# Kernel optimization log

Hardware: AMD Instinct MI355X
Metric: run time of the kernel (lower is better)

## Reference

```python
import jax, jax.numpy as jnp
import numpy as np

ALIGN_CORNERS = True
APPLY_SMOOTHSTEP = True

SIZES = [(32, 32, 32), (64, 64, 64), (128, 128, 128), (256, 256, 256)]
FEAT_DIMS = [4, 4, 4, 4]
N_POINTS = 1048576  # 2**20 sample points (e.g. 8192 rays x 128 samples)


def setup_inputs() -> dict:
    key = jax.random.key(0)
    ks = jax.random.split(key, 1 + len(SIZES))
    # grid_sample-style coords in [-1, 1], layout [1, 1, 1, N, 3] (x, y, z)
    grid = jax.random.uniform(ks[0], (1, 1, 1, N_POINTS, 3), dtype=jnp.float32) * 2.0 - 1.0
    inp = {"grid": grid}
    for i, (size, c) in enumerate(zip(SIZES, FEAT_DIMS)):
        # original init: (rand(1,C,1,1,1)*2-1).repeat over spatial; use randn volumes for a
        # non-degenerate baseline (same shapes/math path)
        inp[f"vol{i}"] = jax.random.normal(ks[1 + i], (1, c, *size), dtype=jnp.float32)
    return inp


def _smooth_sample(vol, grid_pts):
    """Trilinear sample with border padding, align_corners=True, smoothstep weights.

    vol: [C, D, H, W]; grid_pts: [P, 3] with (x, y, z) in [-1, 1].
    Returns [C, P].
    """
    C, D, H, W = vol.shape
    # unnormalize (align_corners=True): [-1,1] -> [0, dim-1]; border padding via clip
    x = jnp.clip((grid_pts[:, 0] + 1.0) * 0.5 * (W - 1), 0.0, W - 1)
    y = jnp.clip((grid_pts[:, 1] + 1.0) * 0.5 * (H - 1), 0.0, H - 1)
    z = jnp.clip((grid_pts[:, 2] + 1.0) * 0.5 * (D - 1), 0.0, D - 1)

    x0 = jnp.floor(x); y0 = jnp.floor(y); z0 = jnp.floor(z)
    tx = x - x0; ty = y - y0; tz = z - z0
    if APPLY_SMOOTHSTEP:
        tx = tx * tx * (3.0 - 2.0 * tx)
        ty = ty * ty * (3.0 - 2.0 * ty)
        tz = tz * tz * (3.0 - 2.0 * tz)

    x0i = x0.astype(jnp.int32); x1i = jnp.minimum(x0i + 1, W - 1)
    y0i = y0.astype(jnp.int32); y1i = jnp.minimum(y0i + 1, H - 1)
    z0i = z0.astype(jnp.int32); z1i = jnp.minimum(z0i + 1, D - 1)

    # 8 corner gathers -> [C, P]
    c000 = vol[:, z0i, y0i, x0i]; c001 = vol[:, z0i, y0i, x1i]
    c010 = vol[:, z0i, y1i, x0i]; c011 = vol[:, z0i, y1i, x1i]
    c100 = vol[:, z1i, y0i, x0i]; c101 = vol[:, z1i, y0i, x1i]
    c110 = vol[:, z1i, y1i, x0i]; c111 = vol[:, z1i, y1i, x1i]

    c00 = c000 + (c001 - c000) * tx
    c01 = c010 + (c011 - c010) * tx
    c10 = c100 + (c101 - c100) * tx
    c11 = c110 + (c111 - c110) * tx
    c0 = c00 + (c01 - c00) * ty
    c1 = c10 + (c11 - c10) * ty
    return c0 + (c1 - c0) * tz


def reference(grid, vol0, vol1, vol2, vol3):
    # grid: [1, 1, 1, N, 3] -> [N, 3]
    pts = grid.reshape(-1, 3)
    n = pts.shape[0]
    out = []
    for vol in (vol0, vol1, vol2, vol3):
        feat = _smooth_sample(vol[0], pts)            # [C, N]
        out.append(feat.reshape(1, -1, 1, 1, n))      # grid_sample output layout
    return jnp.concatenate(out, axis=1)               # [1, sum(C), 1, 1, N]
```

## Files before the change

kernel.cpp:

```cpp
#include <hip/hip_runtime.h>

#define NPTS 1048576
#define NB 32
#define NBINS (NB * NB * NB)

typedef float v4f __attribute__((ext_vector_type(4)));

__device__ __forceinline__ void nt_store4(const float4& f, float4* p) {
    __builtin_nontemporal_store(*(const v4f*)&f, (v4f*)p);
}


__device__ __forceinline__ float4 lerp4(const float4 a, const float4 b, const float t) {
    return make_float4(a.x + (b.x - a.x) * t,
                       a.y + (b.y - a.y) * t,
                       a.z + (b.z - a.z) * t,
                       a.w + (b.w - a.w) * t);
}

struct CoordW { float tx, ty, tz; int b00, b01, b10, b11, x0, x1; };

template<int D>
__device__ __forceinline__ CoordW mkcoord(float gx, float gy, float gz) {
    CoordW c;
    float x = fminf(fmaxf((gx + 1.0f) * (0.5f * (float)(D - 1)), 0.0f), (float)(D - 1));
    float y = fminf(fmaxf((gy + 1.0f) * (0.5f * (float)(D - 1)), 0.0f), (float)(D - 1));
    float z = fminf(fmaxf((gz + 1.0f) * (0.5f * (float)(D - 1)), 0.0f), (float)(D - 1));
    float xf = floorf(x), yf = floorf(y), zf = floorf(z);
    float tx = x - xf, ty = y - yf, tz = z - zf;
    c.tx = tx * tx * (3.0f - 2.0f * tx);
    c.ty = ty * ty * (3.0f - 2.0f * ty);
    c.tz = tz * tz * (3.0f - 2.0f * tz);
    int x0 = (int)xf, y0 = (int)yf, z0 = (int)zf;
    int y1 = min(y0 + 1, D - 1), z1 = min(z0 + 1, D - 1);
    c.x0 = x0;
    c.x1 = min(x0 + 1, D - 1);
    c.b00 = (z0 * D + y0) * D;
    c.b01 = (z0 * D + y1) * D;
    c.b10 = (z1 * D + y0) * D;
    c.b11 = (z1 * D + y1) * D;
    return c;
}

__device__ __forceinline__ float4 reduce8(const float4* q, const CoordW& c) {
    float4 c00 = lerp4(q[0], q[1], c.tx);
    float4 c01 = lerp4(q[2], q[3], c.tx);
    float4 c10 = lerp4(q[4], q[5], c.tx);
    float4 c11 = lerp4(q[6], q[7], c.tx);
    float4 c0 = lerp4(c00, c01, c.ty);
    float4 c1 = lerp4(c10, c11, c.ty);
    return lerp4(c0, c1, c.tz);
}


#define DHW0 (32 * 32 * 32)
#define DHW1 (64 * 64 * 64)
#define DHW2 (128 * 128 * 128)

__global__ __launch_bounds__(256) void xpose_all_kernel(
    const float* __restrict__ v0, const float* __restrict__ v1, const float* __restrict__ v2,
    float4* __restrict__ w0, float4* __restrict__ w1, float4* __restrict__ w2)
{
    constexpr int B2 = DHW2 / 256, B1 = DHW1 / 256;
    int b = blockIdx.x;
    int t = threadIdx.x;
    if (b < B2) {
        int v = b * 256 + t;
        w2[v] = make_float4(v2[v], v2[v + DHW2], v2[v + 2 * DHW2], v2[v + 3 * DHW2]);
    } else if (b < B2 + B1) {
        int v = (b - B2) * 256 + t;
        w1[v] = make_float4(v1[v], v1[v + DHW1], v1[v + 2 * DHW1], v1[v + 3 * DHW1]);
    } else {
        int v = (b - B2 - B1) * 256 + t;
        w0[v] = make_float4(v0[v], v0[v + DHW0], v0[v + 2 * DHW0], v0[v + 3 * DHW0]);
    }
}


__device__ __forceinline__ int bin_of(float gx, float gy, float gz) {
    float ux = fminf(fmaxf((gx + 1.0f) * 0.5f, 0.0f), 1.0f);
    float uy = fminf(fmaxf((gy + 1.0f) * 0.5f, 0.0f), 1.0f);
    float uz = fminf(fmaxf((gz + 1.0f) * 0.5f, 0.0f), 1.0f);
    int bx = min((int)(ux * (float)NB), NB - 1);
    int by = min((int)(uy * (float)NB), NB - 1);
    int bz = min((int)(uz * (float)NB), NB - 1);
    return (bz * NB + by) * NB + bx;
}

__global__ __launch_bounds__(256) void bin_hist_kernel(const float* __restrict__ grid,
                                                       unsigned* __restrict__ hist) {
    int p = blockIdx.x * blockDim.x + threadIdx.x;
    float gx = grid[3 * p + 0];
    float gy = grid[3 * p + 1];
    float gz = grid[3 * p + 2];
    atomicAdd(&hist[bin_of(gx, gy, gz)], 1u);
}

__global__ __launch_bounds__(1024) void scan_kernel(const unsigned* __restrict__ hist,
                                                    unsigned* __restrict__ offsets) {
    __shared__ unsigned partial[1024];
    const int t = threadIdx.x;
    const int base = t * 32;
    unsigned sum = 0;
#pragma unroll
    for (int i = 0; i < 32; ++i) sum += hist[base + i];
    partial[t] = sum;
    __syncthreads();
    for (int off = 1; off < 1024; off <<= 1) {
        unsigned v = (t >= off) ? partial[t - off] : 0u;
        __syncthreads();
        partial[t] += v;
        __syncthreads();
    }
    unsigned run = partial[t] - sum;
#pragma unroll
    for (int i = 0; i < 32; ++i) {
        offsets[base + i] = run;
        run += hist[base + i];
    }
}

__global__ __launch_bounds__(256) void scatter_kernel(const float* __restrict__ grid,
                                                      unsigned* __restrict__ offsets,
                                                      float4* __restrict__ sorted,
                                                      int* __restrict__ inv) {
    int p = blockIdx.x * blockDim.x + threadIdx.x;
    float gx = grid[3 * p + 0];
    float gy = grid[3 * p + 1];
    float gz = grid[3 * p + 2];
    int b = bin_of(gx, gy, gz);
    unsigned pos = atomicAdd(&offsets[b], 1u);
    sorted[pos] = make_float4(gx, gy, gz, __int_as_float(p));
    inv[p] = (int)pos;
}


__global__ __launch_bounds__(256, 4) void gather_sorted_kernel(
    const float4* __restrict__ sorted,
    const float4* __restrict__ w0, const float4* __restrict__ w1,
    const float4* __restrict__ w2, const float* __restrict__ v3,
    float4* __restrict__ wsout)
{
    int bid = blockIdx.x;
    int sb = (bid & 7) * (int)(gridDim.x >> 3) + (bid >> 3);
    int s = sb * 256 + (int)threadIdx.x;
    float4 gp = sorted[s];
    float gx = gp.x, gy = gp.y, gz = gp.z;

    CoordW c0 = mkcoord<32>(gx, gy, gz);
    CoordW c1 = mkcoord<64>(gx, gy, gz);
    CoordW c2 = mkcoord<128>(gx, gy, gz);
    CoordW c3 = mkcoord<256>(gx, gy, gz);

    float4 qa[8], qb[8], qc[8];
    qa[0] = w0[c0.b00 + c0.x0]; qa[1] = w0[c0.b00 + c0.x1];
    qa[2] = w0[c0.b01 + c0.x0]; qa[3] = w0[c0.b01 + c0.x1];
    qa[4] = w0[c0.b10 + c0.x0]; qa[5] = w0[c0.b10 + c0.x1];
    qa[6] = w0[c0.b11 + c0.x0]; qa[7] = w0[c0.b11 + c0.x1];

    qb[0] = w1[c1.b00 + c1.x0]; qb[1] = w1[c1.b00 + c1.x1];
    qb[2] = w1[c1.b01 + c1.x0]; qb[3] = w1[c1.b01 + c1.x1];
    qb[4] = w1[c1.b10 + c1.x0]; qb[5] = w1[c1.b10 + c1.x1];
    qb[6] = w1[c1.b11 + c1.x0]; qb[7] = w1[c1.b11 + c1.x1];

    qc[0] = w2[c2.b00 + c2.x0]; qc[1] = w2[c2.b00 + c2.x1];
    qc[2] = w2[c2.b01 + c2.x0]; qc[3] = w2[c2.b01 + c2.x1];
    qc[4] = w2[c2.b10 + c2.x0]; qc[5] = w2[c2.b10 + c2.x1];
    qc[6] = w2[c2.b11 + c2.x0]; qc[7] = w2[c2.b11 + c2.x1];

    const int xm = min(c3.x0, 254);
    const bool edge = (c3.x0 == 255);
    float2 qd[16];
#pragma unroll
    for (int ch = 0; ch < 4; ++ch) {
        const float* __restrict__ vc = v3 + (size_t)ch * (256 * 256 * 256);
        qd[ch * 4 + 0] = *(const float2*)(vc + c3.b00 + xm);
        qd[ch * 4 + 1] = *(const float2*)(vc + c3.b01 + xm);
        qd[ch * 4 + 2] = *(const float2*)(vc + c3.b10 + xm);
        qd[ch * 4 + 3] = *(const float2*)(vc + c3.b11 + xm);
    }

    float4 f0 = reduce8(qa, c0);
    float4 f1 = reduce8(qb, c1);
    float4 f2 = reduce8(qc, c2);

    float r3[4];
#pragma unroll
    for (int ch = 0; ch < 4; ++ch) {
        float v00a = edge ? qd[ch * 4 + 0].y : qd[ch * 4 + 0].x, v00b = qd[ch * 4 + 0].y;
        float v01a = edge ? qd[ch * 4 + 1].y : qd[ch * 4 + 1].x, v01b = qd[ch * 4 + 1].y;
        float v10a = edge ? qd[ch * 4 + 2].y : qd[ch * 4 + 2].x, v10b = qd[ch * 4 + 2].y;
        float v11a = edge ? qd[ch * 4 + 3].y : qd[ch * 4 + 3].x, v11b = qd[ch * 4 + 3].y;
        float c00 = v00a + (v00b - v00a) * c3.tx;
        float c01 = v01a + (v01b - v01a) * c3.tx;
        float c10 = v10a + (v10b - v10a) * c3.tx;
        float c11 = v11a + (v11b - v11a) * c3.tx;
        float e0 = c00 + (c01 - c00) * c3.ty;
        float e1 = c10 + (c11 - c10) * c3.ty;
        r3[ch] = e0 + (e1 - e0) * c3.tz;
    }
    float4 f3 = make_float4(r3[0], r3[1], r3[2], r3[3]);

    float4* w = wsout + (size_t)s * 4;
    nt_store4(f0, w + 0);
    nt_store4(f1, w + 1);
    nt_store4(f2, w + 2);
    nt_store4(f3, w + 3);
}


__device__ __forceinline__ void permute_one(const float4* __restrict__ wsout,
                                            const int* __restrict__ inv,
                                            float* __restrict__ out, int p) {
    int s = inv[p];
    const float4* w = wsout + (size_t)s * 4;
    float4 f0 = w[0], f1 = w[1], f2 = w[2], f3 = w[3];
    __builtin_nontemporal_store(f0.x, &out[ 0 * NPTS + p]);
    __builtin_nontemporal_store(f0.y, &out[ 1 * NPTS + p]);
    __builtin_nontemporal_store(f0.z, &out[ 2 * NPTS + p]);
    __builtin_nontemporal_store(f0.w, &out[ 3 * NPTS + p]);
    __builtin_nontemporal_store(f1.x, &out[ 4 * NPTS + p]);
    __builtin_nontemporal_store(f1.y, &out[ 5 * NPTS + p]);
    __builtin_nontemporal_store(f1.z, &out[ 6 * NPTS + p]);
    __builtin_nontemporal_store(f1.w, &out[ 7 * NPTS + p]);
    __builtin_nontemporal_store(f2.x, &out[ 8 * NPTS + p]);
    __builtin_nontemporal_store(f2.y, &out[ 9 * NPTS + p]);
    __builtin_nontemporal_store(f2.z, &out[10 * NPTS + p]);
    __builtin_nontemporal_store(f2.w, &out[11 * NPTS + p]);
    __builtin_nontemporal_store(f3.x, &out[12 * NPTS + p]);
    __builtin_nontemporal_store(f3.y, &out[13 * NPTS + p]);
    __builtin_nontemporal_store(f3.z, &out[14 * NPTS + p]);
    __builtin_nontemporal_store(f3.w, &out[15 * NPTS + p]);
}

__global__ __launch_bounds__(256) void permute_kernel(const float4* __restrict__ wsout,
                                                      const int* __restrict__ inv,
                                                      float* __restrict__ out) {
    int p = blockIdx.x * blockDim.x + threadIdx.x;
    permute_one(wsout, inv, out, p);
    permute_one(wsout, inv, out, p + NPTS / 2);
}


template<int D>
__device__ __forceinline__ float4 sample_inter(const float4* __restrict__ v,
                                               float gx, float gy, float gz) {
    CoordW c = mkcoord<D>(gx, gy, gz);
    float4 q[8];
    q[0] = v[c.b00 + c.x0]; q[1] = v[c.b00 + c.x1];
    q[2] = v[c.b01 + c.x0]; q[3] = v[c.b01 + c.x1];
    q[4] = v[c.b10 + c.x0]; q[5] = v[c.b10 + c.x1];
    q[6] = v[c.b11 + c.x0]; q[7] = v[c.b11 + c.x1];
    return reduce8(q, c);
}

template<int D>
__device__ __forceinline__ float4 sample_direct(const float* __restrict__ v,
                                                float gx, float gy, float gz) {
    CoordW c = mkcoord<D>(gx, gy, gz);
    float r[4];
#pragma unroll
    for (int ch = 0; ch < 4; ++ch) {
        const float* __restrict__ vc = v + (size_t)ch * (D * D * D);
        float c000 = vc[c.b00 + c.x0], c001 = vc[c.b00 + c.x1];
        float c010 = vc[c.b01 + c.x0], c011 = vc[c.b01 + c.x1];
        float c100 = vc[c.b10 + c.x0], c101 = vc[c.b10 + c.x1];
        float c110 = vc[c.b11 + c.x0], c111 = vc[c.b11 + c.x1];
        float c00 = c000 + (c001 - c000) * c.tx;
        float c01 = c010 + (c011 - c010) * c.tx;
        float c10 = c100 + (c101 - c100) * c.tx;
        float c11 = c110 + (c111 - c110) * c.tx;
        float e0 = c00 + (c01 - c00) * c.ty;
        float e1 = c10 + (c11 - c10) * c.ty;
        r[ch] = e0 + (e1 - e0) * c.tz;
    }
    return make_float4(r[0], r[1], r[2], r[3]);
}

__global__ __launch_bounds__(256) void mg_direct_kernel(
    const float* __restrict__ grid,
    const float* __restrict__ v0, const float* __restrict__ v1,
    const float* __restrict__ v2, const float* __restrict__ v3,
    float* __restrict__ out)
{
    int p = blockIdx.x * blockDim.x + threadIdx.x;
    float gx = grid[3 * p + 0];
    float gy = grid[3 * p + 1];
    float gz = grid[3 * p + 2];
    float4 f0 = sample_direct<32>(v0, gx, gy, gz);
    float4 f1 = sample_direct<64>(v1, gx, gy, gz);
    float4 f2 = sample_direct<128>(v2, gx, gy, gz);
    float4 f3 = sample_direct<256>(v3, gx, gy, gz);
    out[ 0 * NPTS + p] = f0.x; out[ 1 * NPTS + p] = f0.y;
    out[ 2 * NPTS + p] = f0.z; out[ 3 * NPTS + p] = f0.w;
    out[ 4 * NPTS + p] = f1.x; out[ 5 * NPTS + p] = f1.y;
    out[ 6 * NPTS + p] = f1.z; out[ 7 * NPTS + p] = f1.w;
    out[ 8 * NPTS + p] = f2.x; out[ 9 * NPTS + p] = f2.y;
    out[10 * NPTS + p] = f2.z; out[11 * NPTS + p] = f2.w;
    out[12 * NPTS + p] = f3.x; out[13 * NPTS + p] = f3.y;
    out[14 * NPTS + p] = f3.z; out[15 * NPTS + p] = f3.w;
}

__global__ __launch_bounds__(256) void mg_inter_kernel(
    const float* __restrict__ grid,
    const float4* __restrict__ w0, const float4* __restrict__ w1,
    const float4* __restrict__ w2, const float* __restrict__ v3,
    float* __restrict__ out)
{
    int p = blockIdx.x * blockDim.x + threadIdx.x;
    float gx = grid[3 * p + 0];
    float gy = grid[3 * p + 1];
    float gz = grid[3 * p + 2];
    float4 f0 = sample_inter<32>(w0, gx, gy, gz);
    float4 f1 = sample_inter<64>(w1, gx, gy, gz);
    float4 f2 = sample_inter<128>(w2, gx, gy, gz);
    float4 f3 = sample_direct<256>(v3, gx, gy, gz);
    out[ 0 * NPTS + p] = f0.x; out[ 1 * NPTS + p] = f0.y;
    out[ 2 * NPTS + p] = f0.z; out[ 3 * NPTS + p] = f0.w;
    out[ 4 * NPTS + p] = f1.x; out[ 5 * NPTS + p] = f1.y;
    out[ 6 * NPTS + p] = f1.z; out[ 7 * NPTS + p] = f1.w;
    out[ 8 * NPTS + p] = f2.x; out[ 9 * NPTS + p] = f2.y;
    out[10 * NPTS + p] = f2.z; out[11 * NPTS + p] = f2.w;
    out[12 * NPTS + p] = f3.x; out[13 * NPTS + p] = f3.y;
    out[14 * NPTS + p] = f3.z; out[15 * NPTS + p] = f3.w;
}


extern "C" void kernel_launch(void* const* d_in, const int* in_sizes, int n_in,
                              void* d_out, int out_size, void* d_ws, size_t ws_size,
                              hipStream_t stream) {
    const float* grid = (const float*)d_in[0];
    const float* v0   = (const float*)d_in[1];
    const float* v1   = (const float*)d_in[2];
    const float* v2   = (const float*)d_in[3];
    const float* v3   = (const float*)d_in[4];
    float* out = (float*)d_out;

    constexpr size_t OFF_WSOUT  = 0;
    constexpr size_t OFF_SORTED = OFF_WSOUT  + (size_t)NPTS * 64;
    constexpr size_t OFF_W2     = OFF_SORTED + (size_t)NPTS * 16;
    constexpr size_t OFF_W1     = OFF_W2     + (size_t)DHW2 * 16;
    constexpr size_t OFF_W0     = OFF_W1     + (size_t)DHW1 * 16;
    constexpr size_t OFF_INV    = OFF_W0     + (size_t)DHW0 * 16;
    constexpr size_t OFF_HIST   = OFF_INV    + (size_t)NPTS * 4;
    constexpr size_t OFF_OFFS   = OFF_HIST   + (size_t)NBINS * 4;
    constexpr size_t WS_FULL    = OFF_OFFS   + (size_t)NBINS * 4;
    constexpr size_t WS_INTER   = (size_t)(DHW0 + DHW1 + DHW2) * 16;

    const int threads = 256;
    const int pt_blocks = NPTS / threads;
    char* ws = (char*)d_ws;

    if (ws_size >= WS_FULL) {
        float4*   wsout  = (float4*)(ws + OFF_WSOUT);
        float4*   sorted = (float4*)(ws + OFF_SORTED);
        float4*   w2     = (float4*)(ws + OFF_W2);
        float4*   w1     = (float4*)(ws + OFF_W1);
        float4*   w0     = (float4*)(ws + OFF_W0);
        int*      inv    = (int*)   (ws + OFF_INV);
        unsigned* hist   = (unsigned*)(ws + OFF_HIST);
        unsigned* offs   = (unsigned*)(ws + OFF_OFFS);

        (void)hipMemsetAsync(hist, 0, (size_t)NBINS * 4, stream);
        xpose_all_kernel<<<(DHW0 + DHW1 + DHW2) / threads, threads, 0, stream>>>(
            v0, v1, v2, w0, w1, w2);
        bin_hist_kernel<<<pt_blocks, threads, 0, stream>>>(grid, hist);
        scan_kernel<<<1, 1024, 0, stream>>>(hist, offs);
        scatter_kernel<<<pt_blocks, threads, 0, stream>>>(grid, offs, sorted, inv);
        gather_sorted_kernel<<<pt_blocks, threads, 0, stream>>>(sorted, w0, w1, w2, v3, wsout);
        permute_kernel<<<pt_blocks / 2, threads, 0, stream>>>(wsout, inv, out);
    } else if (ws_size >= WS_INTER) {
        float4* w0 = (float4*)d_ws;
        float4* w1 = w0 + DHW0;
        float4* w2 = w1 + DHW1;
        xpose_all_kernel<<<(DHW0 + DHW1 + DHW2) / threads, threads, 0, stream>>>(
            v0, v1, v2, w0, w1, w2);
        mg_inter_kernel<<<pt_blocks, threads, 0, stream>>>(grid, w0, w1, w2, v3, out);
    } else {
        mg_direct_kernel<<<pt_blocks, threads, 0, stream>>>(grid, v0, v1, v2, v3, out);
    }
}
```

Measured before the change: 662.8 us.

## Fuse transpose with histogram, split gather output into per-level SoA buffers

Merges the volume transpose and point histogram kernels into one launch to cut a kernel launch and let the two independent workloads overlap. The gather kernel now writes each level's float4 into a separate structure-of-arrays buffer right after its reduction, with a scheduling barrier placed after all loads, and its occupancy hint drops from 4 to 3 waves. The permute kernel issues both points' inv and workspace loads before any stores. These changes aim to cut launch overhead and improve memory-level parallelism, at the cost of higher register pressure and less coalesced per-level reads in the permute.

```diff
diff --git a/kernel.cpp b/kernel.cpp
--- a/kernel.cpp
+++ b/kernel.cpp
@@ -3,6 +3,10 @@
 #define NPTS 1048576
 #define NB 32
 #define NBINS (NB * NB * NB)
+
+#define DHW0 (32 * 32 * 32)
+#define DHW1 (64 * 64 * 64)
+#define DHW2 (128 * 128 * 128)
 
 typedef float v4f __attribute__((ext_vector_type(4)));
 
@@ -53,15 +57,23 @@
 }
 
 
-#define DHW0 (32 * 32 * 32)
-#define DHW1 (64 * 64 * 64)
-#define DHW2 (128 * 128 * 128)
-
-__global__ __launch_bounds__(256) void xpose_all_kernel(
+__device__ __forceinline__ int bin_of(float gx, float gy, float gz) {
+    float ux = fminf(fmaxf((gx + 1.0f) * 0.5f, 0.0f), 1.0f);
+    float uy = fminf(fmaxf((gy + 1.0f) * 0.5f, 0.0f), 1.0f);
+    float uz = fminf(fmaxf((gz + 1.0f) * 0.5f, 0.0f), 1.0f);
+    int bx = min((int)(ux * (float)NB), NB - 1);
+    int by = min((int)(uy * (float)NB), NB - 1);
+    int bz = min((int)(uz * (float)NB), NB - 1);
+    return (bz * NB + by) * NB + bx;
+}
+
+
+__global__ __launch_bounds__(256) void xpose_hist_kernel(
     const float* __restrict__ v0, const float* __restrict__ v1, const float* __restrict__ v2,
-    float4* __restrict__ w0, float4* __restrict__ w1, float4* __restrict__ w2)
+    float4* __restrict__ w0, float4* __restrict__ w1, float4* __restrict__ w2,
+    const float* __restrict__ grid, unsigned* __restrict__ hist)
 {
-    constexpr int B2 = DHW2 / 256, B1 = DHW1 / 256;
+    constexpr int B2 = DHW2 / 256, B1 = DHW1 / 256, B0 = DHW0 / 256;
     int b = blockIdx.x;
     int t = threadIdx.x;
     if (b < B2) {
@@ -70,30 +82,16 @@
     } else if (b < B2 + B1) {
         int v = (b - B2) * 256 + t;
         w1[v] = make_float4(v1[v], v1[v + DHW1], v1[v + 2 * DHW1], v1[v + 3 * DHW1]);
-    } else {
+    } else if (b < B2 + B1 + B0) {
         int v = (b - B2 - B1) * 256 + t;
         w0[v] = make_float4(v0[v], v0[v + DHW0], v0[v + 2 * DHW0], v0[v + 3 * DHW0]);
-    }
-}
-
-
-__device__ __forceinline__ int bin_of(float gx, float gy, float gz) {
-    float ux = fminf(fmaxf((gx + 1.0f) * 0.5f, 0.0f), 1.0f);
-    float uy = fminf(fmaxf((gy + 1.0f) * 0.5f, 0.0f), 1.0f);
-    float uz = fminf(fmaxf((gz + 1.0f) * 0.5f, 0.0f), 1.0f);
-    int bx = min((int)(ux * (float)NB), NB - 1);
-    int by = min((int)(uy * (float)NB), NB - 1);
-    int bz = min((int)(uz * (float)NB), NB - 1);
-    return (bz * NB + by) * NB + bx;
-}
-
-__global__ __launch_bounds__(256) void bin_hist_kernel(const float* __restrict__ grid,
-                                                       unsigned* __restrict__ hist) {
-    int p = blockIdx.x * blockDim.x + threadIdx.x;
-    float gx = grid[3 * p + 0];
-    float gy = grid[3 * p + 1];
-    float gz = grid[3 * p + 2];
-    atomicAdd(&hist[bin_of(gx, gy, gz)], 1u);
+    } else {
+        int p = (b - B2 - B1 - B0) * 256 + t;
+        float gx = grid[3 * p + 0];
+        float gy = grid[3 * p + 1];
+        float gz = grid[3 * p + 2];
+        atomicAdd(&hist[bin_of(gx, gy, gz)], 1u);
+    }
 }
 
 __global__ __launch_bounds__(1024) void scan_kernel(const unsigned* __restrict__ hist,
@@ -135,11 +133,12 @@
 }
 
 
-__global__ __launch_bounds__(256, 4) void gather_sorted_kernel(
+__global__ __launch_bounds__(256, 3) void gather_sorted_kernel(
     const float4* __restrict__ sorted,
     const float4* __restrict__ w0, const float4* __restrict__ w1,
     const float4* __restrict__ w2, const float* __restrict__ v3,
-    float4* __restrict__ wsout)
+    float4* __restrict__ ws0, float4* __restrict__ ws1,
+    float4* __restrict__ ws2, float4* __restrict__ ws3)
 {
     int bid = blockIdx.x;
     int sb = (bid & 7) * (int)(gridDim.x >> 3) + (bid >> 3);
@@ -151,8 +150,12 @@
     CoordW c1 = mkcoord<64>(gx, gy, gz);
     CoordW c2 = mkcoord<128>(gx, gy, gz);
     CoordW c3 = mkcoord<256>(gx, gy, gz);
+    const int xm = min(c3.x0, 254);
+    const bool edge = (c3.x0 == 255);
 
     float4 qa[8], qb[8], qc[8];
+    float2 qd[16];
+
     qa[0] = w0[c0.b00 + c0.x0]; qa[1] = w0[c0.b00 + c0.x1];
     qa[2] = w0[c0.b01 + c0.x0]; qa[3] = w0[c0.b01 + c0.x1];
     qa[4] = w0[c0.b10 + c0.x0]; qa[5] = w0[c0.b10 + c0.x1];
@@ -168,9 +171,6 @@
     qc[4] = w2[c2.b10 + c2.x0]; qc[5] = w2[c2.b10 + c2.x1];
     qc[6] = w2[c2.b11 + c2.x0]; qc[7] = w2[c2.b11 + c2.x1];
 
-    const int xm = min(c3.x0, 254);
-    const bool edge = (c3.x0 == 255);
-    float2 qd[16];
 #pragma unroll
     for (int ch = 0; ch < 4; ++ch) {
         const float* __restrict__ vc = v3 + (size_t)ch * (256 * 256 * 256);
@@ -180,9 +180,14 @@
         qd[ch * 4 + 3] = *(const float2*)(vc + c3.b11 + xm);
     }
 
+    __builtin_amdgcn_sched_barrier(0);
+
     float4 f0 = reduce8(qa, c0);
+    nt_store4(f0, ws0 + s);
     float4 f1 = reduce8(qb, c1);
+    nt_store4(f1, ws1 + s);
     float4 f2 = reduce8(qc, c2);
+    nt_store4(f2, ws2 + s);
 
     float r3[4];
 #pragma unroll
@@ -200,21 +205,16 @@
         r3[ch] = e0 + (e1 - e0) * c3.tz;
     }
     float4 f3 = make_float4(r3[0], r3[1], r3[2], r3[3]);
-
-    float4* w = wsout + (size_t)s * 4;
-    nt_store4(f0, w + 0);
-    nt_store4(f1, w + 1);
-    nt_store4(f2, w + 2);
-    nt_store4(f3, w + 3);
-}
-
-
-__device__ __forceinline__ void permute_one(const float4* __restrict__ wsout,
-                                            const int* __restrict__ inv,
-                                            float* __restrict__ out, int p) {
-    int s = inv[p];
-    const float4* w = wsout + (size_t)s * 4;
-    float4 f0 = w[0], f1 = w[1], f2 = w[2], f3 = w[3];
+    nt_store4(f3, ws3 + s);
+}
+
+
+__device__ __forceinline__ void permute_one(const float4* __restrict__ ws0,
+                                            const float4* __restrict__ ws1,
+                                            const float4* __restrict__ ws2,
+                                            const float4* __restrict__ ws3,
+                                            int s, float* __restrict__ out, int p) {
+    float4 f0 = ws0[s], f1 = ws1[s], f2 = ws2[s], f3 = ws3[s];
     __builtin_nontemporal_store(f0.x, &out[ 0 * NPTS + p]);
     __builtin_nontemporal_store(f0.y, &out[ 1 * NPTS + p]);
     __builtin_nontemporal_store(f0.z, &out[ 2 * NPTS + p]);
@@ -233,12 +233,56 @@
     __builtin_nontemporal_store(f3.w, &out[15 * NPTS + p]);
 }
 
-__global__ __launch_bounds__(256) void permute_kernel(const float4* __restrict__ wsout,
-                                                      const int* __restrict__ inv,
-                                                      float* __restrict__ out) {
+__global__ __launch_bounds__(256) void permute_kernel(
+    const float4* __restrict__ ws0, const float4* __restrict__ ws1,
+    const float4* __restrict__ ws2, const float4* __restrict__ ws3,
+    const int* __restrict__ inv, float* __restrict__ out) {
     int p = blockIdx.x * blockDim.x + threadIdx.x;
-    permute_one(wsout, inv, out, p);
-    permute_one(wsout, inv, out, p + NPTS / 2);
+    int sA = inv[p];
+    int sB = inv[p + NPTS / 2];
+    float4 a0 = ws0[sA], a1 = ws1[sA], a2 = ws2[sA], a3 = ws3[sA];
+    float4 b0 = ws0[sB], b1 = ws1[sB], b2 = ws2[sB], b3 = ws3[sB];
+    __builtin_amdgcn_sched_barrier(0);
+    {
+        float4 f0 = a0, f1 = a1, f2 = a2, f3 = a3;
+        int q = p;
+        __builtin_nontemporal_store(f0.x, &out[ 0 * NPTS + q]);
+        __builtin_nontemporal_store(f0.y, &out[ 1 * NPTS + q]);
+        __builtin_nontemporal_store(f0.z, &out[ 2 * NPTS + q]);
+        __builtin_nontemporal_store(f0.w, &out[ 3 * NPTS + q]);
+        __builtin_nontemporal_store(f1.x, &out[ 4 * NPTS + q]);
+        __builtin_nontemporal_store(f1.y, &out[ 5 * NPTS + q]);
+        __builtin_nontemporal_store(f1.z, &out[ 6 * NPTS + q]);
+        __builtin_nontemporal_store(f1.w, &out[ 7 * NPTS + q]);
+        __builtin_nontemporal_store(f2.x, &out[ 8 * NPTS + q]);
+        __builtin_nontemporal_store(f2.y, &out[ 9 * NPTS + q]);
+        __builtin_nontemporal_store(f2.z, &out[10 * NPTS + q]);
+        __builtin_nontemporal_store(f2.w, &out[11 * NPTS + q]);
+        __builtin_nontemporal_store(f3.x, &out[12 * NPTS + q]);
+        __builtin_nontemporal_store(f3.y, &out[13 * NPTS + q]);
+        __builtin_nontemporal_store(f3.z, &out[14 * NPTS + q]);
+        __builtin_nontemporal_store(f3.w, &out[15 * NPTS + q]);
+    }
+    {
+        float4 f0 = b0, f1 = b1, f2 = b2, f3 = b3;
+        int q = p + NPTS / 2;
+        __builtin_nontemporal_store(f0.x, &out[ 0 * NPTS + q]);
+        __builtin_nontemporal_store(f0.y, &out[ 1 * NPTS + q]);
+        __builtin_nontemporal_store(f0.z, &out[ 2 * NPTS + q]);
+        __builtin_nontemporal_store(f0.w, &out[ 3 * NPTS + q]);
+        __builtin_nontemporal_store(f1.x, &out[ 4 * NPTS + q]);
+        __builtin_nontemporal_store(f1.y, &out[ 5 * NPTS + q]);
+        __builtin_nontemporal_store(f1.z, &out[ 6 * NPTS + q]);
+        __builtin_nontemporal_store(f1.w, &out[ 7 * NPTS + q]);
+        __builtin_nontemporal_store(f2.x, &out[ 8 * NPTS + q]);
+        __builtin_nontemporal_store(f2.y, &out[ 9 * NPTS + q]);
+        __builtin_nontemporal_store(f2.z, &out[10 * NPTS + q]);
+        __builtin_nontemporal_store(f2.w, &out[11 * NPTS + q]);
+        __builtin_nontemporal_store(f3.x, &out[12 * NPTS + q]);
+        __builtin_nontemporal_store(f3.y, &out[13 * NPTS + q]);
+        __builtin_nontemporal_store(f3.z, &out[14 * NPTS + q]);
+        __builtin_nontemporal_store(f3.w, &out[15 * NPTS + q]);
+    }
 }
 
 
@@ -352,7 +396,10 @@
     char* ws = (char*)d_ws;
 
     if (ws_size >= WS_FULL) {
-        float4*   wsout  = (float4*)(ws + OFF_WSOUT);
+        float4*   ws0    = (float4*)(ws + OFF_WSOUT);
+        float4*   ws1    = ws0 + NPTS;
+        float4*   ws2    = ws0 + 2 * (size_t)NPTS;
+        float4*   ws3    = ws0 + 3 * (size_t)NPTS;
         float4*   sorted = (float4*)(ws + OFF_SORTED);
         float4*   w2     = (float4*)(ws + OFF_W2);
         float4*   w1     = (float4*)(ws + OFF_W1);
@@ -362,19 +409,20 @@
         unsigned* offs   = (unsigned*)(ws + OFF_OFFS);
 
         (void)hipMemsetAsync(hist, 0, (size_t)NBINS * 4, stream);
-        xpose_all_kernel<<<(DHW0 + DHW1 + DHW2) / threads, threads, 0, stream>>>(
-            v0, v1, v2, w0, w1, w2);
-        bin_hist_kernel<<<pt_blocks, threads, 0, stream>>>(grid, hist);
+        const int xh_blocks = (DHW0 + DHW1 + DHW2) / threads + pt_blocks;
+        xpose_hist_kernel<<<xh_blocks, threads, 0, stream>>>(
+            v0, v1, v2, w0, w1, w2, grid, hist);
         scan_kernel<<<1, 1024, 0, stream>>>(hist, offs);
         scatter_kernel<<<pt_blocks, threads, 0, stream>>>(grid, offs, sorted, inv);
-        gather_sorted_kernel<<<pt_blocks, threads, 0, stream>>>(sorted, w0, w1, w2, v3, wsout);
-        permute_kernel<<<pt_blocks / 2, threads, 0, stream>>>(wsout, inv, out);
+        gather_sorted_kernel<<<pt_blocks, threads, 0, stream>>>(
+            sorted, w0, w1, w2, v3, ws0, ws1, ws2, ws3);
+        permute_kernel<<<pt_blocks / 2, threads, 0, stream>>>(ws0, ws1, ws2, ws3, inv, out);
     } else if (ws_size >= WS_INTER) {
         float4* w0 = (float4*)d_ws;
         float4* w1 = w0 + DHW0;
         float4* w2 = w1 + DHW1;
-        xpose_all_kernel<<<(DHW0 + DHW1 + DHW2) / threads, threads, 0, stream>>>(
-            v0, v1, v2, w0, w1, w2);
+        xpose_hist_kernel<<<(DHW0 + DHW1 + DHW2) / threads, threads, 0, stream>>>(
+            v0, v1, v2, w0, w1, w2, grid, (unsigned*)nullptr);
         mg_inter_kernel<<<pt_blocks, threads, 0, stream>>>(grid, w0, w1, w2, v3, out);
     } else {
         mg_direct_kernel<<<pt_blocks, threads, 0, stream>>>(grid, v0, v1, v2, v3, out);
```

Result: slower. 680.6 us (+2.7%).
